# Kernel optimization log

Hardware: AMD Instinct MI355X
Metric: run time of the kernel (lower is better)

The kernel has to match this reference:

```python
import jax, jax.numpy as jnp
import numpy as np

N_NODES = 100000
N_EDGES = 1600000
D_IN = 100      # entity/relation embedding dim (rel_weight is [100,50])
D_HID = 50      # conv1 out_channels (hard-coded in ctor)
N_REL = 237     # relation_num; rel_embedding doubled -> 474 relation types
N_REL2 = 2 * N_REL
N_BASES = 5     # num_bases hard-coded
N_CLASS = 50    # class_num


def setup_inputs() -> dict:
    key = jax.random.key(0)
    ks = jax.random.split(key, 12)
    x = jax.random.normal(ks[0], (N_NODES, D_IN), dtype=jnp.float32)
    edge_index = jax.random.randint(ks[1], (2, N_EDGES), 0, N_NODES)
    edge_type = jax.random.randint(ks[2], (N_EDGES,), 0, N_REL2)
    rel_embedding = jax.random.normal(ks[3], (N_REL, D_IN), dtype=jnp.float32) * 0.1
    rel_weight = jax.random.uniform(ks[4], (D_IN, D_HID), dtype=jnp.float32)  # nn.Parameter(torch.rand)
    basis1 = jax.random.normal(ks[5], (N_BASES, D_IN, D_HID), dtype=jnp.float32) * 0.1
    comp1 = jax.random.normal(ks[6], (N_REL2, N_BASES), dtype=jnp.float32) * 0.1
    root1 = jax.random.normal(ks[7], (D_IN, D_HID), dtype=jnp.float32) * 0.1
    bias1 = jnp.zeros((D_HID,), dtype=jnp.float32)
    basis2 = jax.random.normal(ks[8], (N_BASES, D_HID, N_CLASS), dtype=jnp.float32) * 0.1
    comp2 = jax.random.normal(ks[9], (N_REL2, N_BASES), dtype=jnp.float32) * 0.1
    root2 = jax.random.normal(ks[10], (D_HID, N_CLASS), dtype=jnp.float32) * 0.1
    bias2 = jnp.zeros((N_CLASS,), dtype=jnp.float32)
    return {
        "x": x, "edge_index": edge_index, "edge_type": edge_type, "target_node": 5,
        "rel_embedding": rel_embedding, "rel_weight": rel_weight,
        "basis1": basis1, "comp1": comp1, "root1": root1, "bias1": bias1,
        "basis2": basis2, "comp2": comp2, "root2": root2, "bias2": bias2,
    }


def _transe_conv(x, src, dst, e_emb, comp_e, basis, root_w, bias):
    """RGCN-style conv with TransE compose and basis decomposition.
    x: [N, Fin], e_emb: [E, Fin], comp_e: [E, B], basis: [B, Fin, Fout].
    message m = x[src] + e_emb; out_e = m @ (sum_b comp_e[b] * basis[b]); mean-agg at dst.
    """
    m = x[src] + e_emb  # [E, Fin] -- dominant gather
    acc = jnp.zeros((m.shape[0], basis.shape[2]), dtype=m.dtype)
    for b in range(basis.shape[0]):  # small fixed basis count (5)
        acc = acc + comp_e[:, b:b + 1] * (m @ basis[b])
    agg = jax.ops.segment_sum(acc, dst, num_segments=x.shape[0])  # [N, Fout]
    cnt = jax.ops.segment_sum(jnp.ones((dst.shape[0],), dtype=x.dtype), dst,
                              num_segments=x.shape[0])
    mean = agg / jnp.maximum(cnt, 1.0)[:, None]
    return mean + x @ root_w + bias


def reference(x, edge_index, edge_type, target_node, rel_embedding, rel_weight,
              basis1, comp1, root1, bias1, basis2, comp2, root2, bias2):
    # x[target_node] = 0
    x = x.at[target_node].set(0.0)
    src, dst = edge_index[0], edge_index[1]
    # rel_embedding doubled (forward + inverse relations)
    rel_full = jnp.concatenate([rel_embedding, rel_embedding], axis=0)  # [2R, D_IN]
    e1 = rel_full[edge_type]                                            # [E, D_IN]
    h = _transe_conv(x, src, dst, e1, comp1[edge_type], basis1, root1, bias1)
    rel2 = rel_full @ rel_weight                                        # [2R, D_HID]
    e2 = rel2[edge_type]                                                # [E, D_HID]
    h = _transe_conv(h, src, dst, e2, comp2[edge_type], basis2, root2, bias2)
    return jax.nn.log_softmax(h, axis=1)
```

## Files before the change

### kernel.cpp

```cpp
#include <hip/hip_runtime.h>
#include <hip/hip_bf16.h>

typedef __hip_bfloat16 bf16;

#define N_NODES 100000
#define N_EDGES 1600000
#define D_IN    100
#define D_HID   50
#define N_REL   237
#define N_REL2  474
#define N_CLASS 50

#define O_RELEMB 0
#define O_RELW   23700
#define O_BASIS1 28700
#define O_COMP1  53700
#define O_ROOT1  56070
#define O_BIAS1  61070
#define O_BASIS2 61120
#define O_COMP2  73620
#define O_ROOT2  75990
#define O_BIAS2  78490
#define W_TOTAL  78540

#define NBUCK    196
#define BSHIFT   9
#define BCAP     10240
#define BIN_EPB  1024
#define BIN_BLKS ((N_EDGES + BIN_EPB - 1) / BIN_EPB)

#define P1_CVTX_BLKS 12500
#define P1_CVTW_BLKS 307
#define P1_TOTAL (P1_CVTX_BLKS + P1_CVTW_BLKS + BIN_BLKS)

#define P2_PACK1_BLKS 160
#define P2_PACK2_BLKS 80
#define P2_REL_BLKS   474
#define P2_TOTAL (P2_PACK1_BLKS + P2_PACK2_BLKS + P2_REL_BLKS)

#define RED_BLKS (N_NODES / 8)

typedef __attribute__((ext_vector_type(8))) short short8;
typedef __attribute__((ext_vector_type(4))) short s16x4;
typedef __attribute__((ext_vector_type(4))) float f32x4;
typedef __attribute__((ext_vector_type(2))) float f32x2;

__device__ __forceinline__ float b2f(bf16 v) { return __bfloat162float(v); }
__device__ __forceinline__ bf16  f2b(float v) { return __float2bfloat16(v); }

#if __has_builtin(__builtin_amdgcn_cvt_f32_fp8) && __has_builtin(__builtin_amdgcn_cvt_pk_fp8_f32)
#define F8_HW 1
#endif
#if __has_builtin(__builtin_amdgcn_cvt_pk_f32_fp8)
#define F8PK_HW 1
#endif

__device__ __forceinline__ float f8tof(unsigned u) {
#ifdef F8_HW
    return __builtin_amdgcn_cvt_f32_fp8((int)u, 0);
#else
    unsigned s = u >> 7, e = (u >> 3) & 0xF, m = u & 7;
    float v;
    if (e == 0) v = (float)m * 0.001953125f;
    else        v = (float)(8 + m) * __builtin_ldexpf(1.f, (int)e - 10);
    return s ? -v : v;
#endif
}

#ifdef F8_HW
#define F8SEL(u, s) __builtin_amdgcn_cvt_f32_fp8((int)(u), (s))
#else
#define F8SEL(u, s) f8tof(((u) >> (8 * (s))) & 0xFFu)
#endif

template <bool HI>
__device__ __forceinline__ f32x2 f8pk(unsigned u) {
#ifdef F8PK_HW
    return __builtin_amdgcn_cvt_pk_f32_fp8((int)u, HI);
#else
    f32x2 r;
    r.x = F8SEL(u, HI ? 2 : 0);
    r.y = F8SEL(u, HI ? 3 : 1);
    return r;
#endif
}

__device__ __forceinline__ unsigned f8enc_sw(float v) {
    unsigned bits = __float_as_uint(v);
    unsigned s = bits >> 31;
    float a = fabsf(v);
    if (a < 0.0009765625f) return s << 7;
    if (a >= 448.f) return (s << 7) | 0x7E;
    int E = (int)((bits >> 23) & 0xFF) - 127;
    unsigned m = bits & 0x7FFFFF;
    if (E < -6) {
        int q = (int)rintf(a * 512.f);
        if (q > 7) q = 7;
        return (s << 7) | (unsigned)q;
    }
    unsigned lsb = (m >> 20) & 1, rnd = (m >> 19) & 1;
    unsigned sticky = (m & 0x7FFFF) ? 1u : 0u;
    unsigned m3 = (m >> 20) + (rnd & (sticky | lsb));
    if (m3 == 8) { m3 = 0; E += 1; }
    if (E > 8) return (s << 7) | 0x7E;
    return (s << 7) | ((unsigned)(E + 7) << 3) | m3;
}

__device__ __forceinline__ unsigned pk4_f8(float v0, float v1, float v2, float v3) {
#ifdef F8_HW
    int p = __builtin_amdgcn_cvt_pk_fp8_f32(v0, v1, 0, false);
    p = __builtin_amdgcn_cvt_pk_fp8_f32(v2, v3, p, true);
    return (unsigned)p;
#else
    return f8enc_sw(v0) | (f8enc_sw(v1) << 8) | (f8enc_sw(v2) << 16) | (f8enc_sw(v3) << 24);
#endif
}

__global__ void k_detect(const unsigned short* __restrict__ xr, int* __restrict__ flag) {
    int tid = threadIdx.x;
    int cnt = 0;
    for (int i = tid; i < 4096; i += 256) {
        unsigned short u = xr[2 * i];
        unsigned e = (u >> 7) & 0xFF;
        bool pl = (e >= 107 && e <= 132) || ((u & 0x7FFF) == 0);
        cnt += pl ? 1 : 0;
    }
    __shared__ int sh[256];
    sh[tid] = cnt;
    __syncthreads();
    for (int s = 128; s > 0; s >>= 1) {
        if (tid < s) sh[tid] += sh[tid + s];
        __syncthreads();
    }
    if (tid == 0) flag[0] = (sh[0] >= 3072) ? 1 : 0;
}

struct WPtrs { const void* p[10]; };

__device__ __forceinline__ void job_bin(int blk, const int* __restrict__ src,
                                        const int* __restrict__ dst,
                                        const int* __restrict__ et,
                                        unsigned* __restrict__ bucketFill,
                                        unsigned long long* __restrict__ staging) {
    __shared__ unsigned lhist[NBUCK];
    __shared__ unsigned lstart[NBUCK];
    __shared__ unsigned gbase[NBUCK];
    __shared__ unsigned scan_tmp[NBUCK];
    __shared__ unsigned long long lval[BIN_EPB];
    __shared__ unsigned ltgt[BIN_EPB];
    int tid = threadIdx.x;
    int base = blk * BIN_EPB;
    int n = N_EDGES - base; if (n > BIN_EPB) n = BIN_EPB;

    for (int i = tid; i < NBUCK; i += 256) lhist[i] = 0;
    __syncthreads();

    unsigned bb[4], rr[4];
    unsigned long long vv[4];
#pragma unroll
    for (int j = 0; j < 4; ++j) {
        int i = j * 256 + tid;
        bb[j] = 0xFFFFFFFFu;
        if (i < n) {
            int e = base + i;
            unsigned d = (unsigned)dst[e];
            unsigned b = d >> BSHIFT;
            bb[j] = b;
            rr[j] = atomicAdd(&lhist[b], 1u);
            vv[j] = ((unsigned long long)d << 32) |
                    (unsigned long long)((unsigned)src[e] | ((unsigned)et[e] << 17));
        }
    }
    __syncthreads();
    unsigned v0 = (tid < NBUCK) ? lhist[tid] : 0;
    if (tid < NBUCK) scan_tmp[tid] = v0;
    __syncthreads();
    for (int s = 1; s < NBUCK; s <<= 1) {
        unsigned t = 0;
        if (tid < NBUCK && tid >= (unsigned)s) t = scan_tmp[tid - s];
        __syncthreads();
        if (tid < NBUCK) scan_tmp[tid] += t;
        __syncthreads();
    }
    if (tid < NBUCK) {
        lstart[tid] = scan_tmp[tid] - v0;
        gbase[tid] = (v0 > 0) ? atomicAdd(&bucketFill[tid], v0) : 0u;
    }
    __syncthreads();
#pragma unroll
    for (int j = 0; j < 4; ++j) {
        if (bb[j] != 0xFFFFFFFFu) {
            unsigned pos = lstart[bb[j]] + rr[j];
            unsigned off = gbase[bb[j]] + rr[j];
            lval[pos] = vv[j];
            ltgt[pos] = (off < BCAP) ? (bb[j] * BCAP + off) : 0xFFFFFFFFu;
        }
    }
    __syncthreads();
    for (int i = tid; i < n; i += 256) {
        unsigned t = ltgt[i];
        if (t != 0xFFFFFFFFu) staging[t] = lval[i];
    }
}

__global__ __launch_bounds__(256) void k_prep1(const void* __restrict__ xr,
                                               const int* __restrict__ flag,
                                               bf16* __restrict__ xc,
                                               WPtrs wp, float* __restrict__ wc,
                                               const int* __restrict__ srcp,
                                               const int* __restrict__ dstp,
                                               const int* __restrict__ etp,
                                               unsigned* __restrict__ bucketFill,
                                               unsigned long long* __restrict__ staging) {
    int blk = blockIdx.x;
    if (blk < P1_CVTX_BLKS) {
        int g = blk * 256 + threadIdx.x;
        int row = g >> 5, c4 = (g & 31) << 2;
        s16x4 o = (s16x4){0, 0, 0, 0};
        if (c4 < 100) {
            if (flag[0]) {
                o = *(const s16x4*)((const unsigned short*)xr + (size_t)row * 100 + c4);
            } else {
                const float* xp = (const float*)xr + (size_t)row * 100 + c4;
                float4 v = *(const float4*)xp;
                bf16 b0 = f2b(v.x), b1 = f2b(v.y), b2 = f2b(v.z), b3 = f2b(v.w);
                o.x = *(short*)&b0; o.y = *(short*)&b1;
                o.z = *(short*)&b2; o.w = *(short*)&b3;
            }
        }
        *(s16x4*)(&xc[(size_t)row * 128 + c4]) = o;
        return;
    }
    blk -= P1_CVTX_BLKS;
    if (blk < P1_CVTW_BLKS) {
        const int sz[10] = {23700, 5000, 25000, 2370, 5000, 50, 12500, 2370, 2500, 50};
        int g = blk * 256 + threadIdx.x;
        if (g >= W_TOTAL) return;
        int j = 0, base = 0;
        while (j < 9 && g >= base + sz[j]) { base += sz[j]; ++j; }
        int idx = g - base;
        float v;
        if (flag[0]) v = b2f(((const bf16*)wp.p[j])[idx]);
        else         v = ((const float*)wp.p[j])[idx];
        wc[g] = v;
        return;
    }
    blk -= P1_CVTW_BLKS;
    job_bin(blk, srcp, dstp, etp, bucketFill, staging);
}

__global__ __launch_bounds__(1024) void k_bucket(const unsigned long long* __restrict__ staging,
                                                 const unsigned* __restrict__ bucketFill,
                                                 int* __restrict__ offs,
                                                 unsigned* __restrict__ se) {
    __shared__ unsigned hist[512];
    __shared__ unsigned excl[512];
    __shared__ unsigned bfs[NBUCK];
    int tid = threadIdx.x;
    int b = blockIdx.x;

    if (tid < NBUCK) {
        unsigned c = bucketFill[tid];
        bfs[tid] = (c > BCAP) ? BCAP : c;
    }
    if (tid < 512) hist[tid] = 0;
    __syncthreads();
    for (int s = 1; s < NBUCK; s <<= 1) {
        unsigned t = 0;
        if (tid < NBUCK && tid >= (unsigned)s) t = bfs[tid - s];
        __syncthreads();
        if (tid < NBUCK) bfs[tid] += t;
        __syncthreads();
    }
    unsigned base = (b == 0) ? 0u : bfs[b - 1];
    unsigned cnt = bfs[b] - base;

    const unsigned long long* p = staging + (size_t)b * BCAP;
    for (unsigned i = tid; i < cnt; i += 1024) {
        unsigned d = (unsigned)(p[i] >> 32);
        atomicAdd(&hist[d & 511], 1u);
    }
    __syncthreads();
    if (tid < 512) excl[tid] = hist[tid];
    __syncthreads();
    for (int s = 1; s < 512; s <<= 1) {
        unsigned t = 0;
        if (tid < 512 && tid >= s) t = excl[tid - s];
        __syncthreads();
        if (tid < 512) excl[tid] += t;
        __syncthreads();
    }
    unsigned my_excl = 0;
    if (tid < 512) my_excl = excl[tid] - hist[tid];
    __syncthreads();
    if (tid < 512) {
        excl[tid] = my_excl;
        hist[tid] = 0;
    }
    __syncthreads();

    if (tid < 512) {
        int node = b * 512 + tid;
        if (node < N_NODES) offs[node] = (int)(base + my_excl);
        if (node == N_NODES - 1) offs[N_NODES] = (int)(base + cnt);
    }

    for (unsigned i = tid; i < cnt; i += 1024) {
        unsigned long long v = p[i];
        unsigned ld = ((unsigned)(v >> 32)) & 511u;
        unsigned r = atomicAdd(&hist[ld], 1u);
        se[base + excl[ld] + r] = (unsigned)v;
    }
}

__device__ __forceinline__ void job_pack(int blk, const float* basis, const float* root,
                                         bf16* Wb, int KL) {
    int g = blk * 256 + threadIdx.x;
    int ks = g / 10240;
    int r = g - ks * 10240;
    int ct = r >> 9;
    int r2 = r & 511;
    int l = r2 >> 3, j = r2 & 7;
    int k = ks * 32 + ((l >> 4) << 3) + j;
    int n = ct * 16 + (l & 15);
    float v = 0.f;
    if (k < KL && n < 300) {
        if (n < 250) { int b = n / 50, f = n - b * 50; v = basis[(b * KL + k) * 50 + f]; }
        else         v = root[k * 50 + (n - 250)];
    }
    Wb[g] = f2b(v);
}

__global__ __launch_bounds__(256) void k_prep2(const float* __restrict__ wc,
                                               bf16* __restrict__ Wb1, bf16* __restrict__ Wb2,
                                               float* __restrict__ rt1, float* __restrict__ rt2,
                                               float* __restrict__ c81, float* __restrict__ c82) {
    int blk = blockIdx.x;
    if (blk < P2_PACK1_BLKS) { job_pack(blk, wc + O_BASIS1, wc + O_ROOT1, Wb1, D_IN); return; }
    blk -= P2_PACK1_BLKS;
    if (blk < P2_PACK2_BLKS) { job_pack(blk, wc + O_BASIS2, wc + O_ROOT2, Wb2, D_HID); return; }
    blk -= P2_PACK2_BLKS;
    {
        const float* rel_emb = wc + O_RELEMB;
        const float* rel_w   = wc + O_RELW;
        const float* basis1  = wc + O_BASIS1;
        const float* comp1   = wc + O_COMP1;
        const float* basis2  = wc + O_BASIS2;
        const float* comp2   = wc + O_COMP2;
        int t = blk;
        int tid = threadIdx.x;
        __shared__ float rf[D_IN];
        __shared__ float r2s[D_HID];
        int tm = (t >= N_REL) ? t - N_REL : t;
        if (tid < D_IN) rf[tid] = rel_emb[tm * D_IN + tid];
        if (tid < 8) {
            c81[t * 8 + tid] = (tid < 5) ? comp1[t * 5 + tid] : 0.f;
            c82[t * 8 + tid] = (tid < 5) ? comp2[t * 5 + tid] : 0.f;
        }
        __syncthreads();
        if (tid < 50) {
            int f = tid;
            float a = 0.f;
            for (int b = 0; b < 5; ++b) {
                float cb = comp1[t * 5 + b];
                float s = 0.f;
                for (int k = 0; k < D_IN; ++k) s += rf[k] * basis1[(b * D_IN + k) * 50 + f];
                a += cb * s;
            }
            rt1[t * 50 + f] = a;
            float s2 = 0.f;
            for (int k = 0; k < D_IN; ++k) s2 += rf[k] * rel_w[k * 50 + f];
            r2s[f] = s2;
        }
        __syncthreads();
        if (tid < 50) {
            int f = tid;
            float a = 0.f;
            for (int b = 0; b < 5; ++b) {
                float cb = comp2[t * 5 + b];
                float s = 0.f;
                for (int k = 0; k < 50; ++k) s += r2s[k] * basis2[(b * 50 + k) * 50 + f];
                a += cb * s;
            }
            rt2[t * 50 + f] = a;
        }
    }
}

template<int KP, bool ZT>
__global__ __launch_bounds__(256) void k_gemm_mfma(const bf16* __restrict__ X,
                                                   const bf16* __restrict__ Wb,
                                                   unsigned char* __restrict__ Y8,
                                                   bf16* __restrict__ R, int M,
                                                   const int* __restrict__ tgt) {
    __shared__ bf16 smem[64 * 320];
    int tid = threadIdx.x;
    int w = tid >> 6, lane = tid & 63;
    int quad = lane >> 4, cIn = lane & 15;
    int base_row = blockIdx.x * 64;

    const int TOT = 64 * KP / 8;
    for (int i = tid; i < TOT; i += 256) {
        int e8 = i * 8;
        int r = e8 / KP, c = e8 - r * KP;
        int row = base_row + r; if (row > M - 1) row = M - 1;
        *(uint4*)(&smem[r * KP + c]) = *(const uint4*)(&X[(size_t)row * KP + c]);
    }
    __syncthreads();

    f32x4 acc[20];
#pragma unroll
    for (int i = 0; i < 20; ++i) acc[i] = (f32x4){0.f, 0.f, 0.f, 0.f};

#pragma unroll
    for (int ks = 0; ks < KP / 32; ++ks) {
        short8 a = *(const short8*)(&smem[(w * 16 + cIn) * KP + ks * 32 + quad * 8]);
#pragma unroll
        for (int ct = 0; ct < 20; ++ct) {
            short8 b = *(const short8*)(&Wb[(size_t)((ks * 20 + ct) * 64 + lane) * 8]);
            acc[ct] = __builtin_amdgcn_mfma_f32_16x16x32_bf16(a, b, acc[ct], 0, 0, 0);
        }
    }
    __syncthreads();

#pragma unroll
    for (int ct = 0; ct < 20; ++ct)
#pragma unroll
        for (int r = 0; r < 4; ++r)
            smem[(w * 16 + quad * 4 + r) * 320 + ct * 16 + cIn] = f2b(acc[ct][r]);
    __syncthreads();

    int tv = -1;
    if (ZT) tv = tgt[0];
    int valid = M - base_row; if (valid > 64) valid = 64;

    for (int i = tid; i < valid * 64; i += 256) {
        int r = i >> 6, u = i & 63;
        int row = base_row + r;
        unsigned pbits;
        if (u < 50) {
            pbits = pk4_f8(b2f(smem[r * 320 + u]),       b2f(smem[r * 320 + 50 + u]),
                           b2f(smem[r * 320 + 100 + u]), b2f(smem[r * 320 + 150 + u]));
        } else if (u < 63) {
            int fb = (u - 50) * 4;
            float v0 = (fb + 0 < 50) ? b2f(smem[r * 320 + 200 + fb + 0]) : 0.f;
            float v1 = (fb + 1 < 50) ? b2f(smem[r * 320 + 200 + fb + 1]) : 0.f;
            float v2 = (fb + 2 < 50) ? b2f(smem[r * 320 + 200 + fb + 2]) : 0.f;
            float v3 = (fb + 3 < 50) ? b2f(smem[r * 320 + 200 + fb + 3]) : 0.f;
            pbits = pk4_f8(v0, v1, v2, v3);
        } else {
            pbits = 0u;
        }
        if (ZT && row == tv) pbits = 0u;
        *(unsigned*)(Y8 + (size_t)row * 256 + u * 4) = pbits;
    }
    for (int i = tid; i < valid * 32; i += 256) {
        int r = i >> 5, cu = i & 31;
        int row = base_row + r;
        int j0 = cu * 2, j1 = j0 + 1;
        unsigned short ua = (j0 < 50) ? *(const unsigned short*)&smem[r * 320 + 250 + j0] : 0;
        unsigned short ub = (j1 < 50) ? *(const unsigned short*)&smem[r * 320 + 250 + j1] : 0;
        unsigned u = (unsigned)ua | ((unsigned)ub << 16);
        if (ZT && row == tv) u = 0u;
        *(unsigned*)((unsigned short*)R + (size_t)row * 64 + j0) = u;
    }
}

__device__ __forceinline__ void edge_body(unsigned p, int f,
        const unsigned char* __restrict__ Y8,
        const float* __restrict__ c8, const float* __restrict__ rt,
        f32x2& acc2, float& accS) {
    unsigned ps = (unsigned)__builtin_amdgcn_readfirstlane((int)p);
    int s_ = (int)(ps & 0x1FFFFu);
    int t_ = (int)(ps >> 17);
    const unsigned char* yr = Y8 + (size_t)s_ * 256;
    unsigned a4 = *(const unsigned*)(yr + 4 * f);
    float y4 = f8tof(yr[200 + f]);
    const float* cp = c8 + t_ * 8;
    f32x4 c03 = *(const f32x4*)cp;
    float c4 = cp[4];
    float rv = rt[t_ * 50 + f];
    f32x2 y01 = f8pk<false>(a4);
    f32x2 y23 = f8pk<true>(a4);
    f32x2 cA; cA.x = c03.x; cA.y = c03.y;
    f32x2 cB; cB.x = c03.z; cB.y = c03.w;
    acc2 += cA * y01;
    acc2 += cB * y23;
    accS += rv + c4 * y4;
}

__device__ __forceinline__ void pair_reduce(const int* __restrict__ off,
        const unsigned int* __restrict__ se, const float* __restrict__ c8,
        const float* __restrict__ rt, const unsigned char* __restrict__ Y8,
        int rowA, int f, float& outA, float& outB, float& cntA, float& cntB) {
    int e0 = __builtin_amdgcn_readfirstlane(off[rowA]);
    int e1 = __builtin_amdgcn_readfirstlane(off[rowA + 1]);
    int e2 = __builtin_amdgcn_readfirstlane(off[rowA + 2]);
    f32x2 a2A; a2A.x = 0.f; a2A.y = 0.f;
    f32x2 a2B; a2B.x = 0.f; a2B.y = 0.f;
    float sA = 0.f, sB = 0.f;
    int eA = e0, eB = e1;
    while (eA + 4 <= e1 && eB + 4 <= e2) {
        unsigned pA0 = se[eA],     pA1 = se[eA + 1], pA2 = se[eA + 2], pA3 = se[eA + 3];
        unsigned pB0 = se[eB],     pB1 = se[eB + 1], pB2 = se[eB + 2], pB3 = se[eB + 3];
        edge_body(pA0, f, Y8, c8, rt, a2A, sA);
        edge_body(pB0, f, Y8, c8, rt, a2B, sB);
        edge_body(pA1, f, Y8, c8, rt, a2A, sA);
        edge_body(pB1, f, Y8, c8, rt, a2B, sB);
        edge_body(pA2, f, Y8, c8, rt, a2A, sA);
        edge_body(pB2, f, Y8, c8, rt, a2B, sB);
        edge_body(pA3, f, Y8, c8, rt, a2A, sA);
        edge_body(pB3, f, Y8, c8, rt, a2B, sB);
        eA += 4; eB += 4;
    }
    while (eA + 4 <= e1) {
        unsigned p0 = se[eA], p1 = se[eA + 1], p2 = se[eA + 2], p3 = se[eA + 3];
        edge_body(p0, f, Y8, c8, rt, a2A, sA);
        edge_body(p1, f, Y8, c8, rt, a2A, sA);
        edge_body(p2, f, Y8, c8, rt, a2A, sA);
        edge_body(p3, f, Y8, c8, rt, a2A, sA);
        eA += 4;
    }
    while (eB + 4 <= e2) {
        unsigned p0 = se[eB], p1 = se[eB + 1], p2 = se[eB + 2], p3 = se[eB + 3];
        edge_body(p0, f, Y8, c8, rt, a2B, sB);
        edge_body(p1, f, Y8, c8, rt, a2B, sB);
        edge_body(p2, f, Y8, c8, rt, a2B, sB);
        edge_body(p3, f, Y8, c8, rt, a2B, sB);
        eB += 4;
    }
    for (; eA < e1; ++eA) edge_body(se[eA], f, Y8, c8, rt, a2A, sA);
    for (; eB < e2; ++eB) edge_body(se[eB], f, Y8, c8, rt, a2B, sB);
    outA = a2A.x + a2A.y + sA;
    outB = a2B.x + a2B.y + sB;
    float nA = (float)(e1 - e0); cntA = nA > 1.f ? nA : 1.f;
    float nB = (float)(e2 - e1); cntB = nB > 1.f ? nB : 1.f;
}

__global__ __launch_bounds__(256) void k_reduce1(const int* __restrict__ off,
                                                 const unsigned int* __restrict__ se,
                                                 const float* __restrict__ c8,
                                                 const float* __restrict__ rt,
                                                 const unsigned char* __restrict__ Y8,
                                                 const bf16* __restrict__ R,
                                                 const float* __restrict__ bias_,
                                                 bf16* __restrict__ h) {
    int wid = threadIdx.x >> 6, lane = threadIdx.x & 63;
    int rowA = __builtin_amdgcn_readfirstlane(blockIdx.x * 8 + wid * 2);
    int f = (lane < 50) ? lane : 49;
    float accA, accB, cntA, cntB;
    pair_reduce(off, se, c8, rt, Y8, rowA, f, accA, accB, cntA, cntB);
    float bv = bias_[f];
    float vA = accA / cntA + b2f(R[(size_t)rowA * 64 + f]) + bv;
    float vB = accB / cntB + b2f(R[(size_t)(rowA + 1) * 64 + f]) + bv;
    h[(size_t)rowA * 64 + lane]       = f2b(lane < 50 ? vA : 0.f);
    h[(size_t)(rowA + 1) * 64 + lane] = f2b(lane < 50 ? vB : 0.f);
}

__device__ __forceinline__ void softmax_store(float acc, float cnt, int row, int f,
        int lane, const bf16* __restrict__ R, const float* __restrict__ bias_,
        int isbf, void* __restrict__ out) {
    float v = -INFINITY;
    if (lane < 50)
        v = acc / cnt + b2f(R[(size_t)row * 64 + f]) + bias_[f];
    float m = v;
    for (int o = 32; o > 0; o >>= 1) m = fmaxf(m, __shfl_xor(m, o));
    float ex = (lane < 50) ? expf(v - m) : 0.f;
    float s = ex;
    for (int o = 32; o > 0; o >>= 1) s += __shfl_xor(s, o);
    float res = v - m - logf(s);
    if (lane < 50) {
        if (isbf) ((bf16*)out)[row * 50 + f] = f2b(res);
        else      ((float*)out)[row * 50 + f] = res;
    }
}

__global__ __launch_bounds__(256) void k_reduce2(const int* __restrict__ off,
                                                 const unsigned int* __restrict__ se,
                                                 const float* __restrict__ c8,
                                                 const float* __restrict__ rt,
                                                 const unsigned char* __restrict__ Y8,
                                                 const bf16* __restrict__ R,
                                                 const float* __restrict__ bias_,
                                                 const int* __restrict__ flag,
                                                 void* __restrict__ out) {
    int wid = threadIdx.x >> 6, lane = threadIdx.x & 63;
    int rowA = __builtin_amdgcn_readfirstlane(blockIdx.x * 8 + wid * 2);
    int f = (lane < 50) ? lane : 49;
    float accA, accB, cntA, cntB;
    pair_reduce(off, se, c8, rt, Y8, rowA, f, accA, accB, cntA, cntB);
    int isbf = flag[0];
    softmax_store(accA, cntA, rowA, f, lane, R, bias_, isbf, out);
    softmax_store(accB, cntB, rowA + 1, f, lane, R, bias_, isbf, out);
}

extern "C" void kernel_launch(void* const* d_in, const int* in_sizes, int n_in,
                              void* d_out, int out_size, void* d_ws, size_t ws_size,
                              hipStream_t stream) {
    const void* x_raw = d_in[0];
    const int*  ei    = (const int*)d_in[1];
    const int*  et    = (const int*)d_in[2];
    const int*  tgt   = (const int*)d_in[3];

    char* wsp = (char*)d_ws;
    size_t off_b = 0;
    auto alloc = [&](size_t bytes) {
        void* p = wsp + off_b;
        off_b = (off_b + bytes + 255) & ~(size_t)255;
        return p;
    };
    unsigned char* Y8 = (unsigned char*)alloc((size_t)N_NODES * 256);
    bf16*  R    = (bf16*) alloc((size_t)N_NODES * 64 * sizeof(bf16));
    bf16*  xc   = (bf16*) alloc((size_t)N_NODES * 128 * sizeof(bf16));
    bf16*  h    = xc;
    unsigned int* se = (unsigned int*)alloc((size_t)N_EDGES * sizeof(unsigned int));
    unsigned long long* staging = (unsigned long long*)alloc((size_t)NBUCK * BCAP * 8);
    int*   offs = (int*)  alloc((size_t)(N_NODES + 1) * sizeof(int));
    unsigned* bucketFill = (unsigned*)alloc((size_t)NBUCK * sizeof(unsigned));
    float* wc   = (float*)alloc((size_t)W_TOTAL * sizeof(float));
    bf16*  Wb1  = (bf16*) alloc((size_t)40960 * sizeof(bf16));
    bf16*  Wb2  = (bf16*) alloc((size_t)20480 * sizeof(bf16));
    float* rt1  = (float*)alloc((size_t)N_REL2 * 50 * sizeof(float));
    float* rt2  = (float*)alloc((size_t)N_REL2 * 50 * sizeof(float));
    float* c81  = (float*)alloc((size_t)N_REL2 * 8 * sizeof(float));
    float* c82  = (float*)alloc((size_t)N_REL2 * 8 * sizeof(float));
    int*   flag = (int*)  alloc(sizeof(int));

    const int* srcp = ei;
    const int* dstp = ei + N_EDGES;

    hipMemsetAsync(bucketFill, 0, (size_t)NBUCK * sizeof(unsigned), stream);

    WPtrs wp;
    for (int i = 0; i < 10; ++i) wp.p[i] = d_in[4 + i];

    k_detect<<<1, 256, 0, stream>>>((const unsigned short*)x_raw, flag);
    k_prep1<<<P1_TOTAL, 256, 0, stream>>>(x_raw, flag, xc, wp, wc, srcp, dstp, et,
                                          bucketFill, staging);
    k_prep2<<<P2_TOTAL, 256, 0, stream>>>(wc, Wb1, Wb2, rt1, rt2, c81, c82);
    k_bucket<<<NBUCK, 1024, 0, stream>>>(staging, bucketFill, offs, se);

    k_gemm_mfma<128, true><<<(N_NODES + 63) / 64, 256, 0, stream>>>(xc, Wb1, Y8, R, N_NODES, tgt);
    k_reduce1<<<RED_BLKS, 256, 0, stream>>>(offs, se, c81, rt1, Y8, R, wc + O_BIAS1, h);

    k_gemm_mfma<64, false><<<(N_NODES + 63) / 64, 256, 0, stream>>>(h, Wb2, Y8, R, N_NODES, nullptr);
    k_reduce2<<<RED_BLKS, 256, 0, stream>>>(offs, se, c82, rt2, Y8, R, wc + O_BIAS2, flag, d_out);
}
```

Before: 415.8 us.

## Fuse x conversion into GEMM, merge prep kernels, overlap bucket sort with GEMM

The first GEMM now reads the raw input x and converts it to bf16 while loading its tile, so the padded bf16 copy of x is no longer written and read back. The weight-conversion pass is dropped and the small prep jobs read the raw parameters directly with a dtype flag. The edge binning and weight packing are merged into one launch, and the per-bucket CSR sort runs as extra 256-thread blocks appended to the first GEMM grid instead of as a separate 1024-thread kernel. This removes launches and a full pass over x, but the GEMM now does narrower 4-byte loads and the bucket blocks compete with GEMM blocks for the same compute units.

```diff
diff --git a/kernel.cpp b/kernel.cpp
--- a/kernel.cpp
+++ b/kernel.cpp
@@ -11,42 +11,31 @@
 #define N_REL2  474
 #define N_CLASS 50
 
-#define O_RELEMB 0
-#define O_RELW   23700
-#define O_BASIS1 28700
-#define O_COMP1  53700
-#define O_ROOT1  56070
-#define O_BIAS1  61070
-#define O_BASIS2 61120
-#define O_COMP2  73620
-#define O_ROOT2  75990
-#define O_BIAS2  78490
-#define W_TOTAL  78540
-
 #define NBUCK    196
 #define BSHIFT   9
 #define BCAP     10240
 #define BIN_EPB  1024
 #define BIN_BLKS ((N_EDGES + BIN_EPB - 1) / BIN_EPB)
 
-#define P1_CVTX_BLKS 12500
-#define P1_CVTW_BLKS 307
-#define P1_TOTAL (P1_CVTX_BLKS + P1_CVTW_BLKS + BIN_BLKS)
-
-#define P2_PACK1_BLKS 160
-#define P2_PACK2_BLKS 80
-#define P2_REL_BLKS   474
-#define P2_TOTAL (P2_PACK1_BLKS + P2_PACK2_BLKS + P2_REL_BLKS)
+#define MID_PACK1_BLKS 160
+#define MID_PACK2_BLKS 80
+#define MID_REL_BLKS   474
+#define MID_TOTAL (BIN_BLKS + MID_PACK1_BLKS + MID_PACK2_BLKS + MID_REL_BLKS)
+
+#define GEMM_BLKS ((N_NODES + 63) / 64)
 
 #define RED_BLKS (N_NODES / 8)
 
 typedef __attribute__((ext_vector_type(8))) short short8;
-typedef __attribute__((ext_vector_type(4))) short s16x4;
 typedef __attribute__((ext_vector_type(4))) float f32x4;
 typedef __attribute__((ext_vector_type(2))) float f32x2;
 
 __device__ __forceinline__ float b2f(bf16 v) { return __bfloat162float(v); }
 __device__ __forceinline__ bf16  f2b(float v) { return __float2bfloat16(v); }
+
+__device__ __forceinline__ float ldw(const void* p, int idx, int isbf) {
+    return isbf ? b2f(((const bf16*)p)[idx]) : ((const float*)p)[idx];
+}
 
 #if __has_builtin(__builtin_amdgcn_cvt_f32_fp8) && __has_builtin(__builtin_amdgcn_cvt_pk_fp8_f32)
 #define F8_HW 1
@@ -134,8 +123,6 @@
     }
     if (tid == 0) flag[0] = (sh[0] >= 3072) ? 1 : 0;
 }
-
-struct WPtrs { const void* p[10]; };
 
 __device__ __forceinline__ void job_bin(int blk, const int* __restrict__ src,
                                         const int* __restrict__ dst,
@@ -203,118 +190,8 @@
     }
 }
 
-__global__ __launch_bounds__(256) void k_prep1(const void* __restrict__ xr,
-                                               const int* __restrict__ flag,
-                                               bf16* __restrict__ xc,
-                                               WPtrs wp, float* __restrict__ wc,
-                                               const int* __restrict__ srcp,
-                                               const int* __restrict__ dstp,
-                                               const int* __restrict__ etp,
-                                               unsigned* __restrict__ bucketFill,
-                                               unsigned long long* __restrict__ staging) {
-    int blk = blockIdx.x;
-    if (blk < P1_CVTX_BLKS) {
-        int g = blk * 256 + threadIdx.x;
-        int row = g >> 5, c4 = (g & 31) << 2;
-        s16x4 o = (s16x4){0, 0, 0, 0};
-        if (c4 < 100) {
-            if (flag[0]) {
-                o = *(const s16x4*)((const unsigned short*)xr + (size_t)row * 100 + c4);
-            } else {
-                const float* xp = (const float*)xr + (size_t)row * 100 + c4;
-                float4 v = *(const float4*)xp;
-                bf16 b0 = f2b(v.x), b1 = f2b(v.y), b2 = f2b(v.z), b3 = f2b(v.w);
-                o.x = *(short*)&b0; o.y = *(short*)&b1;
-                o.z = *(short*)&b2; o.w = *(short*)&b3;
-            }
-        }
-        *(s16x4*)(&xc[(size_t)row * 128 + c4]) = o;
-        return;
-    }
-    blk -= P1_CVTX_BLKS;
-    if (blk < P1_CVTW_BLKS) {
-        const int sz[10] = {23700, 5000, 25000, 2370, 5000, 50, 12500, 2370, 2500, 50};
-        int g = blk * 256 + threadIdx.x;
-        if (g >= W_TOTAL) return;
-        int j = 0, base = 0;
-        while (j < 9 && g >= base + sz[j]) { base += sz[j]; ++j; }
-        int idx = g - base;
-        float v;
-        if (flag[0]) v = b2f(((const bf16*)wp.p[j])[idx]);
-        else         v = ((const float*)wp.p[j])[idx];
-        wc[g] = v;
-        return;
-    }
-    blk -= P1_CVTW_BLKS;
-    job_bin(blk, srcp, dstp, etp, bucketFill, staging);
-}
-
-__global__ __launch_bounds__(1024) void k_bucket(const unsigned long long* __restrict__ staging,
-                                                 const unsigned* __restrict__ bucketFill,
-                                                 int* __restrict__ offs,
-                                                 unsigned* __restrict__ se) {
-    __shared__ unsigned hist[512];
-    __shared__ unsigned excl[512];
-    __shared__ unsigned bfs[NBUCK];
-    int tid = threadIdx.x;
-    int b = blockIdx.x;
-
-    if (tid < NBUCK) {
-        unsigned c = bucketFill[tid];
-        bfs[tid] = (c > BCAP) ? BCAP : c;
-    }
-    if (tid < 512) hist[tid] = 0;
-    __syncthreads();
-    for (int s = 1; s < NBUCK; s <<= 1) {
-        unsigned t = 0;
-        if (tid < NBUCK && tid >= (unsigned)s) t = bfs[tid - s];
-        __syncthreads();
-        if (tid < NBUCK) bfs[tid] += t;
-        __syncthreads();
-    }
-    unsigned base = (b == 0) ? 0u : bfs[b - 1];
-    unsigned cnt = bfs[b] - base;
-
-    const unsigned long long* p = staging + (size_t)b * BCAP;
-    for (unsigned i = tid; i < cnt; i += 1024) {
-        unsigned d = (unsigned)(p[i] >> 32);
-        atomicAdd(&hist[d & 511], 1u);
-    }
-    __syncthreads();
-    if (tid < 512) excl[tid] = hist[tid];
-    __syncthreads();
-    for (int s = 1; s < 512; s <<= 1) {
-        unsigned t = 0;
-        if (tid < 512 && tid >= s) t = excl[tid - s];
-        __syncthreads();
-        if (tid < 512) excl[tid] += t;
-        __syncthreads();
-    }
-    unsigned my_excl = 0;
-    if (tid < 512) my_excl = excl[tid] - hist[tid];
-    __syncthreads();
-    if (tid < 512) {
-        excl[tid] = my_excl;
-        hist[tid] = 0;
-    }
-    __syncthreads();
-
-    if (tid < 512) {
-        int node = b * 512 + tid;
-        if (node < N_NODES) offs[node] = (int)(base + my_excl);
-        if (node == N_NODES - 1) offs[N_NODES] = (int)(base + cnt);
-    }
-
-    for (unsigned i = tid; i < cnt; i += 1024) {
-        unsigned long long v = p[i];
-        unsigned ld = ((unsigned)(v >> 32)) & 511u;
-        unsigned r = atomicAdd(&hist[ld], 1u);
-        se[base + excl[ld] + r] = (unsigned)v;
-    }
-}
-
-__device__ __forceinline__ void job_pack(int blk, const float* basis, const float* root,
-                                         bf16* Wb, int KL) {
+__device__ __forceinline__ void job_pack(int blk, const void* basis, const void* root,
+                                         bf16* Wb, int KL, int isbf) {
     int g = blk * 256 + threadIdx.x;
     int ks = g / 10240;
     int r = g - ks * 10240;
@@ -325,86 +202,196 @@
     int n = ct * 16 + (l & 15);
     float v = 0.f;
     if (k < KL && n < 300) {
-        if (n < 250) { int b = n / 50, f = n - b * 50; v = basis[(b * KL + k) * 50 + f]; }
-        else         v = root[k * 50 + (n - 250)];
+        if (n < 250) { int b = n / 50, f = n - b * 50; v = ldw(basis, (b * KL + k) * 50 + f, isbf); }
+        else         v = ldw(root, k * 50 + (n - 250), isbf);
     }
     Wb[g] = f2b(v);
 }
 
-__global__ __launch_bounds__(256) void k_prep2(const float* __restrict__ wc,
-                                               bf16* __restrict__ Wb1, bf16* __restrict__ Wb2,
-                                               float* __restrict__ rt1, float* __restrict__ rt2,
-                                               float* __restrict__ c81, float* __restrict__ c82) {
+template<int ISBF>
+__device__ __forceinline__ void job_rel(int t,
+        const void* __restrict__ rel_emb, const void* __restrict__ rel_w,
+        const void* __restrict__ basis1, const void* __restrict__ comp1,
+        const void* __restrict__ basis2, const void* __restrict__ comp2,
+        float* __restrict__ rt1, float* __restrict__ rt2,
+        float* __restrict__ c81, float* __restrict__ c82) {
+    int tid = threadIdx.x;
+    __shared__ float rf[D_IN];
+    __shared__ float r2s[D_HID];
+    int tm = (t >= N_REL) ? t - N_REL : t;
+    if (tid < D_IN) rf[tid] = ldw(rel_emb, tm * D_IN + tid, ISBF);
+    if (tid < 8) {
+        c81[t * 8 + tid] = (tid < 5) ? ldw(comp1, t * 5 + tid, ISBF) : 0.f;
+        c82[t * 8 + tid] = (tid < 5) ? ldw(comp2, t * 5 + tid, ISBF) : 0.f;
+    }
+    __syncthreads();
+    if (tid < 50) {
+        int f = tid;
+        float a = 0.f;
+        for (int b = 0; b < 5; ++b) {
+            float cb = ldw(comp1, t * 5 + b, ISBF);
+            float s = 0.f;
+            for (int k = 0; k < D_IN; ++k) s += rf[k] * ldw(basis1, (b * D_IN + k) * 50 + f, ISBF);
+            a += cb * s;
+        }
+        rt1[t * 50 + f] = a;
+        float s2 = 0.f;
+        for (int k = 0; k < D_IN; ++k) s2 += rf[k] * ldw(rel_w, k * 50 + f, ISBF);
+        r2s[f] = s2;
+    }
+    __syncthreads();
+    if (tid < 50) {
+        int f = tid;
+        float a = 0.f;
+        for (int b = 0; b < 5; ++b) {
+            float cb = ldw(comp2, t * 5 + b, ISBF);
+            float s = 0.f;
+            for (int k = 0; k < 50; ++k) s += r2s[k] * ldw(basis2, (b * 50 + k) * 50 + f, ISBF);
+            a += cb * s;
+        }
+        rt2[t * 50 + f] = a;
+    }
+}
+
+__global__ __launch_bounds__(256) void k_mid(const int* __restrict__ srcp,
+                                             const int* __restrict__ dstp,
+                                             const int* __restrict__ etp,
+                                             unsigned* __restrict__ bucketFill,
+                                             unsigned long long* __restrict__ staging,
+                                             const int* __restrict__ flag,
+                                             const void* rel_emb, const void* rel_w,
+                                             const void* basis1, const void* comp1,
+                                             const void* root1,
+                                             const void* basis2, const void* comp2,
+                                             const void* root2,
+                                             bf16* __restrict__ Wb1, bf16* __restrict__ Wb2,
+                                             float* __restrict__ rt1, float* __restrict__ rt2,
+                                             float* __restrict__ c81, float* __restrict__ c82) {
     int blk = blockIdx.x;
-    if (blk < P2_PACK1_BLKS) { job_pack(blk, wc + O_BASIS1, wc + O_ROOT1, Wb1, D_IN); return; }
-    blk -= P2_PACK1_BLKS;
-    if (blk < P2_PACK2_BLKS) { job_pack(blk, wc + O_BASIS2, wc + O_ROOT2, Wb2, D_HID); return; }
-    blk -= P2_PACK2_BLKS;
-    {
-        const float* rel_emb = wc + O_RELEMB;
-        const float* rel_w   = wc + O_RELW;
-        const float* basis1  = wc + O_BASIS1;
-        const float* comp1   = wc + O_COMP1;
-        const float* basis2  = wc + O_BASIS2;
-        const float* comp2   = wc + O_COMP2;
-        int t = blk;
-        int tid = threadIdx.x;
-        __shared__ float rf[D_IN];
-        __shared__ float r2s[D_HID];
-        int tm = (t >= N_REL) ? t - N_REL : t;
-        if (tid < D_IN) rf[tid] = rel_emb[tm * D_IN + tid];
-        if (tid < 8) {
-            c81[t * 8 + tid] = (tid < 5) ? comp1[t * 5 + tid] : 0.f;
-            c82[t * 8 + tid] = (tid < 5) ? comp2[t * 5 + tid] : 0.f;
-        }
+    if (blk < BIN_BLKS) { job_bin(blk, srcp, dstp, etp, bucketFill, staging); return; }
+    blk -= BIN_BLKS;
+    int isbf = flag[0];
+    if (blk < MID_PACK1_BLKS) { job_pack(blk, basis1, root1, Wb1, D_IN, isbf); return; }
+    blk -= MID_PACK1_BLKS;
+    if (blk < MID_PACK2_BLKS) { job_pack(blk, basis2, root2, Wb2, D_HID, isbf); return; }
+    blk -= MID_PACK2_BLKS;
+    if (isbf) job_rel<1>(blk, rel_emb, rel_w, basis1, comp1, basis2, comp2, rt1, rt2, c81, c82);
+    else      job_rel<0>(blk, rel_emb, rel_w, basis1, comp1, basis2, comp2, rt1, rt2, c81, c82);
+}
+
+__device__ __forceinline__ void job_bucket(int b, char* shraw,
+        const unsigned long long* __restrict__ staging,
+        const unsigned* __restrict__ bucketFill,
+        int* __restrict__ offs, unsigned* __restrict__ se) {
+    unsigned* hist = (unsigned*)shraw;
+    unsigned* excl = hist + 512;
+    unsigned* bfs  = excl + 512;
+    unsigned* tmp  = bfs + 256;
+    int tid = threadIdx.x;
+
+    if (tid < NBUCK) {
+        unsigned c = bucketFill[tid];
+        bfs[tid] = (c > BCAP) ? BCAP : c;
+    }
+    hist[tid] = 0; hist[tid + 256] = 0;
+    __syncthreads();
+    for (int s = 1; s < NBUCK; s <<= 1) {
+        unsigned t = 0;
+        if (tid < NBUCK && tid >= s) t = bfs[tid - s];
         __syncthreads();
-        if (tid < 50) {
-            int f = tid;
-            float a = 0.f;
-            for (int b = 0; b < 5; ++b) {
-                float cb = comp1[t * 5 + b];
-                float s = 0.f;
-                for (int k = 0; k < D_IN; ++k) s += rf[k] * basis1[(b * D_IN + k) * 50 + f];
-                a += cb * s;
-            }
-            rt1[t * 50 + f] = a;
-            float s2 = 0.f;
-            for (int k = 0; k < D_IN; ++k) s2 += rf[k] * rel_w[k * 50 + f];
-            r2s[f] = s2;
-        }
+        if (tid < NBUCK) bfs[tid] += t;
         __syncthreads();
-        if (tid < 50) {
-            int f = tid;
-            float a = 0.f;
-            for (int b = 0; b < 5; ++b) {
-                float cb = comp2[t * 5 + b];
-                float s = 0.f;
-                for (int k = 0; k < 50; ++k) s += r2s[k] * basis2[(b * 50 + k) * 50 + f];
-                a += cb * s;
-            }
-            rt2[t * 50 + f] = a;
-        }
-    }
-}
-
-template<int KP, bool ZT>
-__global__ __launch_bounds__(256) void k_gemm_mfma(const bf16* __restrict__ X,
-                                                   const bf16* __restrict__ Wb,
-                                                   unsigned char* __restrict__ Y8,
-                                                   bf16* __restrict__ R, int M,
-                                                   const int* __restrict__ tgt) {
-    __shared__ bf16 smem[64 * 320];
+    }
+    unsigned base = (b == 0) ? 0u : bfs[b - 1];
+    unsigned cnt = bfs[b] - base;
+
+    const unsigned long long* p = staging + (size_t)b * BCAP;
+    for (unsigned i = tid; i < cnt; i += 256) {
+        unsigned d = (unsigned)(p[i] >> 32);
+        atomicAdd(&hist[d & 511], 1u);
+    }
+    __syncthreads();
+    unsigned h0 = hist[2 * tid], h1 = hist[2 * tid + 1];
+    tmp[tid] = h0 + h1;
+    __syncthreads();
+    for (int s = 1; s < 256; s <<= 1) {
+        unsigned t = (tid >= s) ? tmp[tid - s] : 0u;
+        __syncthreads();
+        tmp[tid] += t;
+        __syncthreads();
+    }
+    unsigned pe = (tid > 0) ? tmp[tid - 1] : 0u;
+    excl[2 * tid]     = pe;
+    excl[2 * tid + 1] = pe + h0;
+    hist[2 * tid] = 0; hist[2 * tid + 1] = 0;
+    __syncthreads();
+
+#pragma unroll
+    for (int q = 0; q < 2; ++q) {
+        int li = 2 * tid + q;
+        int node = b * 512 + li;
+        if (node < N_NODES) offs[node] = (int)(base + excl[li]);
+        if (node == N_NODES - 1) offs[N_NODES] = (int)(base + cnt);
+    }
+
+    for (unsigned i = tid; i < cnt; i += 256) {
+        unsigned long long v = p[i];
+        unsigned ld = ((unsigned)(v >> 32)) & 511u;
+        unsigned r = atomicAdd(&hist[ld], 1u);
+        se[base + excl[ld] + r] = (unsigned)v;
+    }
+}
+
+template<int KP, bool ZT, bool RAWX>
+__global__ __launch_bounds__(256) void k_gemm_b(const void* __restrict__ Xraw,
+                                                const int* __restrict__ flag,
+                                                const bf16* __restrict__ Wb,
+                                                unsigned char* __restrict__ Y8,
+                                                bf16* __restrict__ R, int M,
+                                                const int* __restrict__ tgt,
+                                                const unsigned long long* __restrict__ staging,
+                                                const unsigned* __restrict__ bucketFill,
+                                                int* __restrict__ offs,
+                                                unsigned* __restrict__ se,
+                                                int gemmBlks) {
+    __shared__ __attribute__((aligned(16))) char shraw[64 * 320 * 2];
+    if ((int)blockIdx.x >= gemmBlks) {
+        job_bucket(blockIdx.x - gemmBlks, shraw, staging, bucketFill, offs, se);
+        return;
+    }
+    bf16* smem = (bf16*)shraw;
     int tid = threadIdx.x;
     int w = tid >> 6, lane = tid & 63;
     int quad = lane >> 4, cIn = lane & 15;
     int base_row = blockIdx.x * 64;
 
-    const int TOT = 64 * KP / 8;
-    for (int i = tid; i < TOT; i += 256) {
-        int e8 = i * 8;
-        int r = e8 / KP, c = e8 - r * KP;
-        int row = base_row + r; if (row > M - 1) row = M - 1;
-        *(uint4*)(&smem[r * KP + c]) = *(const uint4*)(&X[(size_t)row * KP + c]);
+    if (RAWX) {
+        int isbf = flag[0];
+        for (int i = tid; i < 64 * 64; i += 256) {
+            int r = i >> 6, c2 = (i & 63) << 1;
+            int row = base_row + r; if (row > M - 1) row = M - 1;
+            unsigned pkd = 0;
+            if (c2 < 100) {
+                if (isbf) {
+                    pkd = *(const unsigned*)((const unsigned short*)Xraw + (size_t)row * 100 + c2);
+                } else {
+                    const float* xp = (const float*)Xraw + (size_t)row * 100 + c2;
+                    float vx = xp[0], vy = xp[1];
+                    bf16 b0 = f2b(vx), b1 = f2b(vy);
+                    pkd = (unsigned)*(unsigned short*)&b0 | ((unsigned)*(unsigned short*)&b1 << 16);
+                }
+            }
+            *(unsigned*)(&smem[r * KP + c2]) = pkd;
+        }
+    } else {
+        const bf16* X = (const bf16*)Xraw;
+        const int TOT = 64 * KP / 8;
+        for (int i = tid; i < TOT; i += 256) {
+            int e8 = i * 8;
+            int r = e8 / KP, c = e8 - r * KP;
+            int row = base_row + r; if (row > M - 1) row = M - 1;
+            *(uint4*)(&smem[r * KP + c]) = *(const uint4*)(&X[(size_t)row * KP + c]);
+        }
     }
     __syncthreads();
 
@@ -543,14 +530,15 @@
                                                  const float* __restrict__ rt,
                                                  const unsigned char* __restrict__ Y8,
                                                  const bf16* __restrict__ R,
-                                                 const float* __restrict__ bias_,
+                                                 const void* __restrict__ bias_raw,
+                                                 const int* __restrict__ flag,
                                                  bf16* __restrict__ h) {
     int wid = threadIdx.x >> 6, lane = threadIdx.x & 63;
     int rowA = __builtin_amdgcn_readfirstlane(blockIdx.x * 8 + wid * 2);
     int f = (lane < 50) ? lane : 49;
     float accA, accB, cntA, cntB;
     pair_reduce(off, se, c8, rt, Y8, rowA, f, accA, accB, cntA, cntB);
-    float bv = bias_[f];
+    float bv = ldw(bias_raw, f, flag[0]);
     float vA = accA / cntA + b2f(R[(size_t)rowA * 64 + f]) + bv;
     float vB = accB / cntB + b2f(R[(size_t)(rowA + 1) * 64 + f]) + bv;
     h[(size_t)rowA * 64 + lane]       = f2b(lane < 50 ? vA : 0.f);
@@ -558,11 +546,11 @@
 }
 
 __device__ __forceinline__ void softmax_store(float acc, float cnt, int row, int f,
-        int lane, const bf16* __restrict__ R, const float* __restrict__ bias_,
+        int lane, const bf16* __restrict__ R, float bv,
         int isbf, void* __restrict__ out) {
     float v = -INFINITY;
     if (lane < 50)
-        v = acc / cnt + b2f(R[(size_t)row * 64 + f]) + bias_[f];
+        v = acc / cnt + b2f(R[(size_t)row * 64 + f]) + bv;
     float m = v;
     for (int o = 32; o > 0; o >>= 1) m = fmaxf(m, __shfl_xor(m, o));
     float ex = (lane < 50) ? expf(v - m) : 0.f;
@@ -581,7 +569,7 @@
                                                  const float* __restrict__ rt,
                                                  const unsigned char* __restrict__ Y8,
                                                  const bf16* __restrict__ R,
-                                                 const float* __restrict__ bias_,
+                                                 const void* __restrict__ bias_raw,
                                                  const int* __restrict__ flag,
                                                  void* __restrict__ out) {
     int wid = threadIdx.x >> 6, lane = threadIdx.x & 63;
@@ -590,8 +578,9 @@
     float accA, accB, cntA, cntB;
     pair_reduce(off, se, c8, rt, Y8, rowA, f, accA, accB, cntA, cntB);
     int isbf = flag[0];
-    softmax_store(accA, cntA, rowA, f, lane, R, bias_, isbf, out);
-    softmax_store(accB, cntB, rowA + 1, f, lane, R, bias_, isbf, out);
+    float bv = ldw(bias_raw, f, isbf);
+    softmax_store(accA, cntA, rowA, f, lane, R, bv, isbf, out);
+    softmax_store(accB, cntB, rowA + 1, f, lane, R, bv, isbf, out);
 }
 
 extern "C" void kernel_launch(void* const* d_in, const int* in_sizes, int n_in,
@@ -601,6 +590,16 @@
     const int*  ei    = (const int*)d_in[1];
     const int*  et    = (const int*)d_in[2];
     const int*  tgt   = (const int*)d_in[3];
+    const void* rel_emb = d_in[4];
+    const void* rel_w   = d_in[5];
+    const void* basis1  = d_in[6];
+    const void* comp1   = d_in[7];
+    const void* root1   = d_in[8];
+    const void* bias1   = d_in[9];
+    const void* basis2  = d_in[10];
+    const void* comp2   = d_in[11];
+    const void* root2   = d_in[12];
+    const void* bias2   = d_in[13];
 
     char* wsp = (char*)d_ws;
     size_t off_b = 0;
@@ -611,13 +610,11 @@
     };
     unsigned char* Y8 = (unsigned char*)alloc((size_t)N_NODES * 256);
     bf16*  R    = (bf16*) alloc((size_t)N_NODES * 64 * sizeof(bf16));
-    bf16*  xc   = (bf16*) alloc((size_t)N_NODES * 128 * sizeof(bf16));
-    bf16*  h    = xc;
+    bf16*  h    = (bf16*) alloc((size_t)N_NODES * 64 * sizeof(bf16));
     unsigned int* se = (unsigned int*)alloc((size_t)N_EDGES * sizeof(unsigned int));
     unsigned long long* staging = (unsigned long long*)alloc((size_t)NBUCK * BCAP * 8);
     int*   offs = (int*)  alloc((size_t)(N_NODES + 1) * sizeof(int));
     unsigned* bucketFill = (unsigned*)alloc((size_t)NBUCK * sizeof(unsigned));
-    float* wc   = (float*)alloc((size_t)W_TOTAL * sizeof(float));
     bf16*  Wb1  = (bf16*) alloc((size_t)40960 * sizeof(bf16));
     bf16*  Wb2  = (bf16*) alloc((size_t)20480 * sizeof(bf16));
     float* rt1  = (float*)alloc((size_t)N_REL2 * 50 * sizeof(float));
@@ -631,18 +628,20 @@
 
     hipMemsetAsync(bucketFill, 0, (size_t)NBUCK * sizeof(unsigned), stream);
 
-    WPtrs wp;
-    for (int i = 0; i < 10; ++i) wp.p[i] = d_in[4 + i];
-
     k_detect<<<1, 256, 0, stream>>>((const unsigned short*)x_raw, flag);
-    k_prep1<<<P1_TOTAL, 256, 0, stream>>>(x_raw, flag, xc, wp, wc, srcp, dstp, et,
-                                          bucketFill, staging);
-    k_prep2<<<P2_TOTAL, 256, 0, stream>>>(wc, Wb1, Wb2, rt1, rt2, c81, c82);
-    k_bucket<<<NBUCK, 1024, 0, stream>>>(staging, bucketFill, offs, se);
-
-    k_gemm_mfma<128, true><<<(N_NODES + 63) / 64, 256, 0, stream>>>(xc, Wb1, Y8, R, N_NODES, tgt);
-    k_reduce1<<<RED_BLKS, 256, 0, stream>>>(offs, se, c81, rt1, Y8, R, wc + O_BIAS1, h);
-
-    k_gemm_mfma<64, false><<<(N_NODES + 63) / 64, 256, 0, stream>>>(h, Wb2, Y8, R, N_NODES, nullptr);
-    k_reduce2<<<RED_BLKS, 256, 0, stream>>>(offs, se, c82, rt2, Y8, R, wc + O_BIAS2, flag, d_out);
-}
+
+    k_mid<<<MID_TOTAL, 256, 0, stream>>>(srcp, dstp, et, bucketFill, staging, flag,
+                                         rel_emb, rel_w, basis1, comp1, root1,
+                                         basis2, comp2, root2,
+                                         Wb1, Wb2, rt1, rt2, c81, c82);
+
+    k_gemm_b<128, true, true><<<GEMM_BLKS + NBUCK, 256, 0, stream>>>(
+        x_raw, flag, Wb1, Y8, R, N_NODES, tgt, staging, bucketFill, offs, se, GEMM_BLKS);
+
+    k_reduce1<<<RED_BLKS, 256, 0, stream>>>(offs, se, c81, rt1, Y8, R, bias1, flag, h);
+
+    k_gemm_b<64, false, false><<<GEMM_BLKS, 256, 0, stream>>>(
+        h, flag, Wb2, Y8, R, N_NODES, nullptr, staging, bucketFill, offs, se, GEMM_BLKS);
+
+    k_reduce2<<<RED_BLKS, 256, 0, stream>>>(offs, se, c82, rt2, Y8, R, bias2, flag, d_out);
+}
```

After: 412.2 us. No clear change (-0.9%).
